# Performance work log

Measured on AMD Instinct MI355X. Metric: run time of the kernel, lower is better.

Reference implementation:

```python
import jax, jax.numpy as jnp
import numpy as np

S_DIM, T_DIM, FEAT_DIM = 2048, 2048, 128
NCE_N, NCE_T, NCE_MOM = 16384, 0.07, 0.5
N_DATA, BATCH = 100000, 64
EPS = 1e-7


def _l2norm(x):
    return x / jnp.linalg.norm(x, axis=1, keepdims=True)


def setup_inputs() -> dict:
    key = jax.random.key(0)
    ks = jax.random.split(key, 10)
    feat_s = jax.random.normal(ks[0], (BATCH, S_DIM), dtype=jnp.float32)
    feat_t = jax.random.normal(ks[1], (BATCH, T_DIM), dtype=jnp.float32)
    idx = jax.random.randint(ks[2], (BATCH,), 0, N_DATA)
    sample_idx = jax.random.randint(ks[3], (BATCH, NCE_N + 1), 0, N_DATA)
    sample_idx = sample_idx.at[:, 0].set(idx)  # positive sample in column 0
    # Embed linear weights (Linear(dim_in, feat_dim))
    w_s = jax.random.normal(ks[4], (FEAT_DIM, S_DIM), dtype=jnp.float32) / np.sqrt(S_DIM)
    b_s = jnp.zeros((FEAT_DIM,), dtype=jnp.float32)
    w_t = jax.random.normal(ks[5], (FEAT_DIM, T_DIM), dtype=jnp.float32) / np.sqrt(T_DIM)
    b_t = jnp.zeros((FEAT_DIM,), dtype=jnp.float32)
    # memory banks, uniform(-stdv, stdv), stdv = 1/sqrt(feat_dim/3)
    stdv = 1.0 / np.sqrt(FEAT_DIM / 3.0)
    mem_v1 = jax.random.uniform(ks[6], (N_DATA, FEAT_DIM), dtype=jnp.float32, minval=-stdv, maxval=stdv)
    mem_v2 = jax.random.uniform(ks[7], (N_DATA, FEAT_DIM), dtype=jnp.float32, minval=-stdv, maxval=stdv)
    return {"feat_s": feat_s, "feat_t": feat_t, "idx": idx, "sample_idx": sample_idx,
            "w_s": w_s, "b_s": b_s, "w_t": w_t, "b_t": b_t,
            "mem_v1": mem_v1, "mem_v2": mem_v2}


def _contrast_out(mem, samp_idx, v):
    # gather [B, K+1, D] from memory bank, bmm against [B, D]
    w = mem[samp_idx]                                # [B, K+1, D]
    logits = jnp.einsum('bkd,bd->bk', w, v) / NCE_T  # [B, K+1]
    out = jnp.exp(logits)
    z = jnp.mean(out) * N_DATA                       # first-pass Z estimate
    return out / z


def _contrast_loss(x):
    b = x.shape[0]
    m = float(NCE_N) / N_DATA
    log_d1 = jnp.log(x[:, 0] / (x[:, 0] + m + EPS))          # positives
    log_d0 = jnp.log(m / (x[:, 1:] + m + EPS))               # negatives
    return -(jnp.sum(log_d1) + jnp.sum(log_d0)) / b


def reference(feat_s, feat_t, idx, sample_idx, w_s, b_s, w_t, b_t, mem_v1, mem_v2):
    hs = _l2norm(feat_s @ w_s.T + b_s)  # [B, D]
    ht = _l2norm(feat_t @ w_t.T + b_t)  # [B, D]
    out_s = _contrast_out(mem_v2, sample_idx, hs)  # anchor=student vs teacher memory
    out_t = _contrast_out(mem_v1, sample_idx, ht)  # anchor=teacher vs student memory
    return _contrast_loss(out_s) + _contrast_loss(out_t)
```

## Files before the change

kernel.cpp:

```cpp
#include <hip/hip_runtime.h>

#define DIM_IN   2048
#define FEAT     128
#define KP1      16385
#define NDATA    100000
#define BATCH    64
#define NB       128
#define NBLK     ((NDATA + NB - 1) / NB)
#define GCH      16

constexpr float NCE_T_INV = 1.0f / 0.07f;
constexpr float M_CONST   = 16384.0f / 100000.0f;
constexpr float EPS_C     = 1e-7f;

typedef short bf16x8 __attribute__((ext_vector_type(8)));
typedef float f32x4  __attribute__((ext_vector_type(4)));

#define VP_PLANE 34816
#define VP_SIDE  17408
#define VP_ROW   272

__global__ void __launch_bounds__(1024) embed_kernel(
    const float* __restrict__ feat_s, const float* __restrict__ feat_t,
    const float* __restrict__ w_s, const float* __restrict__ b_s,
    const float* __restrict__ w_t, const float* __restrict__ b_t,
    char* __restrict__ vplanes, float* __restrict__ z_zero,
    float* __restrict__ out_zero)
{
    const int blk  = blockIdx.x;
    const int side = blk >> 6;
    const int b    = blk & 63;
    const float* feat = (side == 0 ? feat_s : feat_t) + (size_t)b * DIM_IN;
    const float* w    = (side == 0 ? w_s : w_t);
    const float* bias = (side == 0 ? b_s : b_t);

    __shared__ float sfeat[DIM_IN];
    __shared__ float pre[FEAT];
    __shared__ float wsum[2];

    const int t = threadIdx.x;
    if (blk == 0) {
        if (t < 128) z_zero[t] = 0.f;
        else if (t == 128) out_zero[0] = 0.f;
    }
    {
        const float4* f4 = (const float4*)feat;
        float4* s4 = (float4*)sfeat;
        if (t < 512) s4[t] = f4[t];
    }
    __syncthreads();

    const int wv = t >> 6, ln = t & 63;
    const float4* w4  = (const float4*)w;
    const float4* sf4 = (const float4*)sfeat;
#pragma unroll 2
    for (int i = 0; i < 8; ++i) {
        const int d = wv + i * 16;
        float s = 0.f;
#pragma unroll
        for (int seg = 0; seg < 8; ++seg) {
            float4 a = w4[d * (DIM_IN / 4) + seg * 64 + ln];
            float4 f = sf4[seg * 64 + ln];
            s += a.x * f.x + a.y * f.y + a.z * f.z + a.w * f.w;
        }
#pragma unroll
        for (int o = 32; o > 0; o >>= 1) s += __shfl_xor(s, o, 64);
        if (ln == 0) pre[d] = s;
    }
    __syncthreads();

    if (t < 128) {
        float p = pre[t] + bias[t];
        pre[t] = p;
        float sq = p * p;
#pragma unroll
        for (int o = 32; o > 0; o >>= 1) sq += __shfl_xor(sq, o, 64);
        if ((t & 63) == 0) wsum[t >> 6] = sq;
    }
    __syncthreads();
    if (t < 128) {
        float inv_norm = 1.0f / sqrtf(wsum[0] + wsum[1]);
        float x = pre[t] * inv_norm;
        unsigned int u = __float_as_uint(x);
        unsigned short h = (unsigned short)(u >> 16);
        float hf = __uint_as_float(u & 0xffff0000u);
        float lr = x - hf;
        unsigned short l = (unsigned short)(__float_as_uint(lr) >> 16);
        const size_t off = (size_t)side * VP_SIDE + (size_t)b * VP_ROW + t * 2;
        *(unsigned short*)(vplanes + off)            = h;
        *(unsigned short*)(vplanes + VP_PLANE + off) = l;
    }
}

__global__ void __launch_bounds__(512) gemm_exp_kernel(
    const float* __restrict__ mem_v1, const float* __restrict__ mem_v2,
    const char* __restrict__ vplanes, float* __restrict__ E)
{
    __shared__ __align__(16) char lds[34816];

    const int bx   = blockIdx.x;
    const int side = bx & 1;
    const int tile = bx >> 1;
    const int n0   = tile * NB;
    const float* bank = (side == 0 ? mem_v2 : mem_v1);
    const int t  = threadIdx.x;
    const int wv = t >> 6, ln = t & 63;
    const int lm = ln & 15;
    const int kb = ln >> 4;
    const int nloc = wv * 16 + lm;

    int rowg = n0 + nloc; if (rowg > NDATA - 1) rowg = NDATA - 1;
    const float* bsrc = bank + (size_t)rowg * FEAT;
    float4 bq[8];
#pragma unroll
    for (int c = 0; c < 4; ++c) {
        const float4* p = (const float4*)(bsrc + c * 32 + kb * 8);
        bq[c * 2 + 0] = p[0];
        bq[c * 2 + 1] = p[1];
    }

    {
        const char* hbase = vplanes + (size_t)side * VP_SIDE;
        const char* lbase = vplanes + VP_PLANE + (size_t)side * VP_SIDE;
        for (int seg = wv; seg < 34; seg += 8) {
            const char* src = (seg < 17 ? hbase + seg * 1024
                                        : lbase + (seg - 17) * 1024) + ln * 16;
            __builtin_amdgcn_global_load_lds(
                (const __attribute__((address_space(1))) void*)src,
                (__attribute__((address_space(3))) void*)(lds + seg * 1024),
                16, 0, 0);
        }
    }

    f32x4 acc[4];
#pragma unroll
    for (int mi = 0; mi < 4; ++mi) acc[mi] = (f32x4){0.f, 0.f, 0.f, 0.f};

    __syncthreads();

#pragma unroll
    for (int c = 0; c < 4; ++c) {
        const float xs[8] = {bq[c*2].x,   bq[c*2].y,   bq[c*2].z,   bq[c*2].w,
                             bq[c*2+1].x, bq[c*2+1].y, bq[c*2+1].z, bq[c*2+1].w};
        bf16x8 bh, bl;
#pragma unroll
        for (int j = 0; j < 8; ++j) {
            unsigned int u = __float_as_uint(xs[j]);
            bh[j] = (short)(u >> 16);
            float hf = __uint_as_float(u & 0xffff0000u);
            bl[j] = (short)(__float_as_uint(xs[j] - hf) >> 16);
        }
        bf16x8 ah[4], al[4];
#pragma unroll
        for (int mi = 0; mi < 4; ++mi) {
            ah[mi] = *(const bf16x8*)(lds + (mi * 16 + lm) * VP_ROW + c * 64 + kb * 16);
            al[mi] = *(const bf16x8*)(lds + 17408 + (mi * 16 + lm) * VP_ROW + c * 64 + kb * 16);
        }
#pragma unroll
        for (int mi = 0; mi < 4; ++mi) {
            acc[mi] = __builtin_amdgcn_mfma_f32_16x16x32_bf16(ah[mi], bh, acc[mi], 0, 0, 0);
            acc[mi] = __builtin_amdgcn_mfma_f32_16x16x32_bf16(al[mi], bh, acc[mi], 0, 0, 0);
            acc[mi] = __builtin_amdgcn_mfma_f32_16x16x32_bf16(ah[mi], bl, acc[mi], 0, 0, 0);
        }
    }

    const int nn = n0 + nloc;
    if (nn < NDATA) {
#pragma unroll
        for (int mi = 0; mi < 4; ++mi)
#pragma unroll
            for (int j = 0; j < 4; ++j) {
                const int anchor = mi * 16 + kb * 4 + j;
                E[(size_t)(side * 64 + anchor) * NDATA + nn] =
                    __expf(acc[mi][j] * NCE_T_INV);
            }
    }
}

__global__ void __launch_bounds__(256) gather_z_kernel(
    const int* __restrict__ sample_idx, const float* __restrict__ E,
    float* __restrict__ ex_out, float* __restrict__ z_out)
{
    const int blk   = blockIdx.x;
    const int chunk = blk >> 7;
    const int sb    = blk & 127;
    const int b     = sb & 63;
    const float* Eb = E + (size_t)sb * NDATA;

    float zp = 0.f;
    for (int k = chunk * 256 + threadIdx.x; k < KP1; k += GCH * 256) {
        const int idx = sample_idx[(size_t)b * KP1 + k];
        const float e = Eb[idx];
        ex_out[(size_t)sb * KP1 + k] = e;
        zp += e;
    }
#pragma unroll
    for (int o = 32; o > 0; o >>= 1) zp += __shfl_xor(zp, o, 64);
    __shared__ float zw[4];
    if ((threadIdx.x & 63) == 0) zw[threadIdx.x >> 6] = zp;
    __syncthreads();
    if (threadIdx.x == 0) atomicAdd(&z_out[sb], zw[0] + zw[1] + zw[2] + zw[3]);
}

__global__ void __launch_bounds__(256) loss_kernel(
    const float* __restrict__ ex_in, const float* __restrict__ z_in,
    float* __restrict__ out)
{
    const int blk   = blockIdx.x;
    const int chunk = blk >> 7;
    const int sb    = blk & 127;
    const int side  = sb >> 6;

    __shared__ float zsh;
    if (threadIdx.x < 64) {
        float zv = z_in[side * 64 + threadIdx.x];
#pragma unroll
        for (int o = 32; o > 0; o >>= 1) zv += __shfl_xor(zv, o, 64);
        if (threadIdx.x == 0) zsh = zv;
    }
    __syncthreads();

    const float z  = zsh * ((float)NDATA / (64.0f * (float)KP1));
    const float rz = 1.0f / z;
    const float* ex = ex_in + (size_t)sb * KP1;

    float part = 0.f;
    for (int k = chunk * 256 + threadIdx.x; k < KP1; k += 512) {
        const float x = ex[k] * rz;
        if (k == 0) part += __logf(x / (x + M_CONST + EPS_C));
        else        part += __logf(M_CONST / (x + M_CONST + EPS_C));
    }
#pragma unroll
    for (int o = 32; o > 0; o >>= 1) part += __shfl_xor(part, o, 64);
    __shared__ float pw[4];
    if ((threadIdx.x & 63) == 0) pw[threadIdx.x >> 6] = part;
    __syncthreads();
    if (threadIdx.x == 0)
        atomicAdd(out, -(pw[0] + pw[1] + pw[2] + pw[3]) * (1.0f / 64.0f));
}

extern "C" void kernel_launch(void* const* d_in, const int* in_sizes, int n_in,
                              void* d_out, int out_size, void* d_ws, size_t ws_size,
                              hipStream_t stream)
{
    const float* feat_s     = (const float*)d_in[0];
    const float* feat_t     = (const float*)d_in[1];
    const int*   sample_idx = (const int*)  d_in[3];
    const float* w_s        = (const float*)d_in[4];
    const float* b_s        = (const float*)d_in[5];
    const float* w_t        = (const float*)d_in[6];
    const float* b_t        = (const float*)d_in[7];
    const float* mem_v1     = (const float*)d_in[8];
    const float* mem_v2     = (const float*)d_in[9];
    float* out = (float*)d_out;

    char*  ws     = (char*)d_ws;
    float* ws_z   = (float*)ws;
    float* ws_ex  = (float*)(ws + 512);
    char*  ws_vp  = (char*)(ws + 512);
    float* ws_E   = (float*)(ws + 512 + (size_t)2 * BATCH * KP1 * sizeof(float));

    embed_kernel<<<2 * BATCH, 1024, 0, stream>>>(feat_s, feat_t, w_s, b_s, w_t, b_t,
                                                 ws_vp, ws_z, out);
    gemm_exp_kernel<<<2 * NBLK, 512, 0, stream>>>(mem_v1, mem_v2, ws_vp, ws_E);
    gather_z_kernel<<<2 * BATCH * GCH, 256, 0, stream>>>(sample_idx, ws_E, ws_ex, ws_z);
    loss_kernel<<<2 * BATCH * 2, 256, 0, stream>>>(ws_ex, ws_z, out);
}
```

Measured before the change: 204.2 us.

## Process two row tiles per GEMM block with software-prefetched bank loads

Each gemm_exp block now handles 256 memory-bank rows instead of 128, reusing the LDS-loaded anchor planes for two sub-tiles. Bank loads are issued three chunks ahead in a rolling register buffer, so global latency overlaps MFMA work, and each sub-tile's exp results are stored as soon as it finishes. The gather and loss kernels are split into more chunks to raise parallelism. The cost is fewer GEMM blocks, more register pressure, and more atomics in the loss kernel.

```diff
diff --git a/kernel.cpp b/kernel.cpp
--- a/kernel.cpp
+++ b/kernel.cpp
@@ -5,9 +5,10 @@
 #define KP1      16385
 #define NDATA    100000
 #define BATCH    64
-#define NB       128
-#define NBLK     ((NDATA + NB - 1) / NB)
-#define GCH      16
+#define NBT      256
+#define NTIL     ((NDATA + NBT - 1) / NBT)
+#define GCH      32
+#define LCH      8
 
 constexpr float NCE_T_INV = 1.0f / 0.07f;
 constexpr float M_CONST   = 16384.0f / 100000.0f;
@@ -101,7 +102,7 @@
     const int bx   = blockIdx.x;
     const int side = bx & 1;
     const int tile = bx >> 1;
-    const int n0   = tile * NB;
+    const int n0   = tile * NBT;
     const float* bank = (side == 0 ? mem_v2 : mem_v1);
     const int t  = threadIdx.x;
     const int wv = t >> 6, ln = t & 63;
@@ -109,14 +110,17 @@
     const int kb = ln >> 4;
     const int nloc = wv * 16 + lm;
 
-    int rowg = n0 + nloc; if (rowg > NDATA - 1) rowg = NDATA - 1;
-    const float* bsrc = bank + (size_t)rowg * FEAT;
-    float4 bq[8];
-#pragma unroll
-    for (int c = 0; c < 4; ++c) {
-        const float4* p = (const float4*)(bsrc + c * 32 + kb * 8);
-        bq[c * 2 + 0] = p[0];
-        bq[c * 2 + 1] = p[1];
+    int r0 = n0 + nloc;        if (r0 > NDATA - 1) r0 = NDATA - 1;
+    int r1 = n0 + 128 + nloc;  if (r1 > NDATA - 1) r1 = NDATA - 1;
+    const float* bs0 = bank + (size_t)r0 * FEAT + kb * 8;
+    const float* bs1 = bank + (size_t)r1 * FEAT + kb * 8;
+
+    float4 bq[4][2];
+#pragma unroll
+    for (int j = 0; j < 3; ++j) {
+        const float4* p = (const float4*)(bs0 + j * 32);
+        bq[j][0] = p[0];
+        bq[j][1] = p[1];
     }
 
     {
@@ -139,16 +143,26 @@
     __syncthreads();
 
 #pragma unroll
-    for (int c = 0; c < 4; ++c) {
-        const float xs[8] = {bq[c*2].x,   bq[c*2].y,   bq[c*2].z,   bq[c*2].w,
-                             bq[c*2+1].x, bq[c*2+1].y, bq[c*2+1].z, bq[c*2+1].w};
+    for (int j = 0; j < 8; ++j) {
+        if (j + 3 < 8) {
+            const int jj = j + 3;
+            const float* p = (jj < 4 ? bs0 : bs1) + (jj & 3) * 32;
+            bq[jj & 3][0] = ((const float4*)p)[0];
+            bq[jj & 3][1] = ((const float4*)p)[1];
+            asm volatile("" ::: "memory");
+        }
+        const int c = j & 3;
+        const float xs[8] = {bq[j & 3][0].x, bq[j & 3][0].y,
+                             bq[j & 3][0].z, bq[j & 3][0].w,
+                             bq[j & 3][1].x, bq[j & 3][1].y,
+                             bq[j & 3][1].z, bq[j & 3][1].w};
         bf16x8 bh, bl;
 #pragma unroll
-        for (int j = 0; j < 8; ++j) {
-            unsigned int u = __float_as_uint(xs[j]);
-            bh[j] = (short)(u >> 16);
+        for (int jj = 0; jj < 8; ++jj) {
+            unsigned int u = __float_as_uint(xs[jj]);
+            bh[jj] = (short)(u >> 16);
             float hf = __uint_as_float(u & 0xffff0000u);
-            bl[j] = (short)(__float_as_uint(xs[j] - hf) >> 16);
+            bl[jj] = (short)(__float_as_uint(xs[jj] - hf) >> 16);
         }
         bf16x8 ah[4], al[4];
 #pragma unroll
@@ -162,18 +176,24 @@
             acc[mi] = __builtin_amdgcn_mfma_f32_16x16x32_bf16(al[mi], bh, acc[mi], 0, 0, 0);
             acc[mi] = __builtin_amdgcn_mfma_f32_16x16x32_bf16(ah[mi], bl, acc[mi], 0, 0, 0);
         }
-    }
-
-    const int nn = n0 + nloc;
-    if (nn < NDATA) {
-#pragma unroll
-        for (int mi = 0; mi < 4; ++mi)
-#pragma unroll
-            for (int j = 0; j < 4; ++j) {
-                const int anchor = mi * 16 + kb * 4 + j;
-                E[(size_t)(side * 64 + anchor) * NDATA + nn] =
-                    __expf(acc[mi][j] * NCE_T_INV);
+        if (c == 3) {
+            const int nn = n0 + (j >> 2) * 128 + nloc;
+            if (nn < NDATA) {
+#pragma unroll
+                for (int mi = 0; mi < 4; ++mi)
+#pragma unroll
+                    for (int jj = 0; jj < 4; ++jj) {
+                        const int anchor = mi * 16 + kb * 4 + jj;
+                        E[(size_t)(side * 64 + anchor) * NDATA + nn] =
+                            __expf(acc[mi][jj] * NCE_T_INV);
+                    }
             }
+            if (j < 7) {
+#pragma unroll
+                for (int mi = 0; mi < 4; ++mi)
+                    acc[mi] = (f32x4){0.f, 0.f, 0.f, 0.f};
+            }
+        }
     }
 }
 
@@ -225,7 +245,7 @@
     const float* ex = ex_in + (size_t)sb * KP1;
 
     float part = 0.f;
-    for (int k = chunk * 256 + threadIdx.x; k < KP1; k += 512) {
+    for (int k = chunk * 256 + threadIdx.x; k < KP1; k += LCH * 256) {
         const float x = ex[k] * rz;
         if (k == 0) part += __logf(x / (x + M_CONST + EPS_C));
         else        part += __logf(M_CONST / (x + M_CONST + EPS_C));
@@ -262,7 +282,7 @@
 
     embed_kernel<<<2 * BATCH, 1024, 0, stream>>>(feat_s, feat_t, w_s, b_s, w_t, b_t,
                                                  ws_vp, ws_z, out);
-    gemm_exp_kernel<<<2 * NBLK, 512, 0, stream>>>(mem_v1, mem_v2, ws_vp, ws_E);
+    gemm_exp_kernel<<<2 * NTIL, 512, 0, stream>>>(mem_v1, mem_v2, ws_vp, ws_E);
     gather_z_kernel<<<2 * BATCH * GCH, 256, 0, stream>>>(sample_idx, ws_E, ws_ex, ws_z);
-    loss_kernel<<<2 * BATCH * 2, 256, 0, stream>>>(ws_ex, ws_z, out);
-}
+    loss_kernel<<<2 * BATCH * LCH, 256, 0, stream>>>(ws_ex, ws_z, out);
+}
```

New measurement: 212.0 us. 3.8% more time.

## Stage memory-bank tile in swizzled LDS with smaller tiles and more grid parallelism

Applied to the files above, without the earlier changes.

The GEMM kernel now processes 64 bank rows per block instead of 128. Waves split the anchor dimension into halves, so each wave keeps two accumulators instead of four. The bank rows are copied asynchronously into XOR-swizzled LDS through global_load_lds, instead of each lane loading float4 directly into registers. The gather and loss kernels are also split into more chunks per row to launch more blocks. This should improve memory-level parallelism and occupancy, at the cost of larger LDS use per block (about 66KB) and reloading the anchor planes into twice as many blocks.

```diff
diff --git a/kernel.cpp b/kernel.cpp
--- a/kernel.cpp
+++ b/kernel.cpp
@@ -5,9 +5,10 @@
 #define KP1      16385
 #define NDATA    100000
 #define BATCH    64
-#define NB       128
-#define NBLK     ((NDATA + NB - 1) / NB)
-#define GCH      16
+#define NBG      64
+#define NTG      ((NDATA + NBG - 1) / NBG)
+#define GCH      32
+#define LCH      8
 
 constexpr float NCE_T_INV = 1.0f / 0.07f;
 constexpr float M_CONST   = 16384.0f / 100000.0f;
@@ -96,29 +97,36 @@
     const float* __restrict__ mem_v1, const float* __restrict__ mem_v2,
     const char* __restrict__ vplanes, float* __restrict__ E)
 {
-    __shared__ __align__(16) char lds[34816];
+    __shared__ __align__(16) char lds[67584];
 
     const int bx   = blockIdx.x;
     const int side = bx & 1;
     const int tile = bx >> 1;
-    const int n0   = tile * NB;
+    const int n0   = tile * NBG;
     const float* bank = (side == 0 ? mem_v2 : mem_v1);
     const int t  = threadIdx.x;
     const int wv = t >> 6, ln = t & 63;
     const int lm = ln & 15;
     const int kb = ln >> 4;
-    const int nloc = wv * 16 + lm;
-
-    int rowg = n0 + nloc; if (rowg > NDATA - 1) rowg = NDATA - 1;
-    const float* bsrc = bank + (size_t)rowg * FEAT;
-    float4 bq[8];
-#pragma unroll
-    for (int c = 0; c < 4; ++c) {
-        const float4* p = (const float4*)(bsrc + c * 32 + kb * 8);
-        bq[c * 2 + 0] = p[0];
-        bq[c * 2 + 1] = p[1];
-    }
-
+    const int ntile = wv & 3;
+    const int mhalf = wv >> 2;
+    const int nloc  = ntile * 16 + lm;
+
+    {
+        const size_t bmax = (size_t)NDATA * 512 - 16;
+        const char* bbase = (const char*)bank;
+        for (int s = wv; s < 32; s += 8) {
+            const int o   = s * 1024 + ln * 16;
+            const int row = o >> 9;
+            const int so  = (o & ~511) | ((o & 511) ^ ((row & 7) << 4));
+            size_t g = (size_t)n0 * 512 + so;
+            if (g > bmax) g = bmax;
+            __builtin_amdgcn_global_load_lds(
+                (const __attribute__((address_space(1))) void*)(bbase + g),
+                (__attribute__((address_space(3))) void*)(lds + 34816 + s * 1024),
+                16, 0, 0);
+        }
+    }
     {
         const char* hbase = vplanes + (size_t)side * VP_SIDE;
         const char* lbase = vplanes + VP_PLANE + (size_t)side * VP_SIDE;
@@ -132,16 +140,19 @@
         }
     }
 
-    f32x4 acc[4];
-#pragma unroll
-    for (int mi = 0; mi < 4; ++mi) acc[mi] = (f32x4){0.f, 0.f, 0.f, 0.f};
-
-    __syncthreads();
-
+    f32x4 acc[2];
+    acc[0] = (f32x4){0.f, 0.f, 0.f, 0.f};
+    acc[1] = (f32x4){0.f, 0.f, 0.f, 0.f};
+
+    __syncthreads();
+
+    const int sw = (nloc & 7) << 4;
 #pragma unroll
     for (int c = 0; c < 4; ++c) {
-        const float xs[8] = {bq[c*2].x,   bq[c*2].y,   bq[c*2].z,   bq[c*2].w,
-                             bq[c*2+1].x, bq[c*2+1].y, bq[c*2+1].z, bq[c*2+1].w};
+        const int bofs = nloc * 512 + c * 128 + kb * 32;
+        const float4 f0 = *(const float4*)(lds + 34816 + ((bofs)      ^ sw));
+        const float4 f1 = *(const float4*)(lds + 34816 + ((bofs + 16) ^ sw));
+        const float xs[8] = {f0.x, f0.y, f0.z, f0.w, f1.x, f1.y, f1.z, f1.w};
         bf16x8 bh, bl;
 #pragma unroll
         for (int j = 0; j < 8; ++j) {
@@ -150,30 +161,29 @@
             float hf = __uint_as_float(u & 0xffff0000u);
             bl[j] = (short)(__float_as_uint(xs[j] - hf) >> 16);
         }
-        bf16x8 ah[4], al[4];
-#pragma unroll
-        for (int mi = 0; mi < 4; ++mi) {
-            ah[mi] = *(const bf16x8*)(lds + (mi * 16 + lm) * VP_ROW + c * 64 + kb * 16);
-            al[mi] = *(const bf16x8*)(lds + 17408 + (mi * 16 + lm) * VP_ROW + c * 64 + kb * 16);
-        }
-#pragma unroll
-        for (int mi = 0; mi < 4; ++mi) {
-            acc[mi] = __builtin_amdgcn_mfma_f32_16x16x32_bf16(ah[mi], bh, acc[mi], 0, 0, 0);
-            acc[mi] = __builtin_amdgcn_mfma_f32_16x16x32_bf16(al[mi], bh, acc[mi], 0, 0, 0);
-            acc[mi] = __builtin_amdgcn_mfma_f32_16x16x32_bf16(ah[mi], bl, acc[mi], 0, 0, 0);
+#pragma unroll
+        for (int i = 0; i < 2; ++i) {
+            const int mi = mhalf * 2 + i;
+            bf16x8 ah = *(const bf16x8*)(lds + (mi * 16 + lm) * VP_ROW + c * 64 + kb * 16);
+            bf16x8 al = *(const bf16x8*)(lds + 17408 + (mi * 16 + lm) * VP_ROW + c * 64 + kb * 16);
+            acc[i] = __builtin_amdgcn_mfma_f32_16x16x32_bf16(ah, bh, acc[i], 0, 0, 0);
+            acc[i] = __builtin_amdgcn_mfma_f32_16x16x32_bf16(al, bh, acc[i], 0, 0, 0);
+            acc[i] = __builtin_amdgcn_mfma_f32_16x16x32_bf16(ah, bl, acc[i], 0, 0, 0);
         }
     }
 
     const int nn = n0 + nloc;
     if (nn < NDATA) {
 #pragma unroll
-        for (int mi = 0; mi < 4; ++mi)
-#pragma unroll
-            for (int j = 0; j < 4; ++j) {
-                const int anchor = mi * 16 + kb * 4 + j;
+        for (int i = 0; i < 2; ++i) {
+            const int mi = mhalf * 2 + i;
+#pragma unroll
+            for (int jj = 0; jj < 4; ++jj) {
+                const int anchor = mi * 16 + kb * 4 + jj;
                 E[(size_t)(side * 64 + anchor) * NDATA + nn] =
-                    __expf(acc[mi][j] * NCE_T_INV);
+                    __expf(acc[i][jj] * NCE_T_INV);
             }
+        }
     }
 }
 
@@ -225,7 +235,7 @@
     const float* ex = ex_in + (size_t)sb * KP1;
 
     float part = 0.f;
-    for (int k = chunk * 256 + threadIdx.x; k < KP1; k += 512) {
+    for (int k = chunk * 256 + threadIdx.x; k < KP1; k += LCH * 256) {
         const float x = ex[k] * rz;
         if (k == 0) part += __logf(x / (x + M_CONST + EPS_C));
         else        part += __logf(M_CONST / (x + M_CONST + EPS_C));
@@ -262,7 +272,7 @@
 
     embed_kernel<<<2 * BATCH, 1024, 0, stream>>>(feat_s, feat_t, w_s, b_s, w_t, b_t,
                                                  ws_vp, ws_z, out);
-    gemm_exp_kernel<<<2 * NBLK, 512, 0, stream>>>(mem_v1, mem_v2, ws_vp, ws_E);
+    gemm_exp_kernel<<<2 * NTG, 512, 0, stream>>>(mem_v1, mem_v2, ws_vp, ws_E);
     gather_z_kernel<<<2 * BATCH * GCH, 256, 0, stream>>>(sample_idx, ws_E, ws_ex, ws_z);
-    loss_kernel<<<2 * BATCH * 2, 256, 0, stream>>>(ws_ex, ws_z, out);
-}
+    loss_kernel<<<2 * BATCH * LCH, 256, 0, stream>>>(ws_ex, ws_z, out);
+}
```

Measured after the change: 205.7 us. About the same (+0.7%).
